# Performance work log

Measured on AMD Instinct MI355X. Metric: run time of the kernel, lower is better.

## Reference

```python
import jax, jax.numpy as jnp
import numpy as np

N_NODES = 30000
N_REL = 200
N_EDGES = 150000
N_EDGES_NHOP = 30000
NFEAT = 100
NHID = 100
REL_DIM = 100
NHEADS = 2
ALPHA = 0.2  # leaky relu slope


def setup_inputs() -> dict:
    key = jax.random.key(0)
    ks = jax.random.split(key, 16)
    s = 0.1
    D = NHEADS * NHID
    inp = {}
    inp["entity_embeddings"] = jax.random.normal(ks[0], (N_NODES, NFEAT), jnp.float32)
    inp["relation_embed"] = jax.random.normal(ks[1], (N_REL, REL_DIM), jnp.float32)
    inp["edge_list"] = jax.random.randint(ks[2], (2, N_EDGES), 0, N_NODES)
    inp["edge_type"] = jax.random.randint(ks[3], (N_EDGES,), 0, N_REL)
    inp["edge_embed"] = jax.random.normal(ks[4], (N_EDGES, REL_DIM), jnp.float32)
    inp["edge_list_nhop"] = jax.random.randint(ks[5], (2, N_EDGES_NHOP), 0, N_NODES)
    inp["edge_type_nhop"] = jax.random.randint(ks[6], (N_EDGES_NHOP, 2), 0, N_REL)
    inp["entity_embeddings_mapping"] = jax.random.normal(ks[7], (N_NODES, NFEAT), jnp.float32)
    # learned params (xavier-like scale)
    inp["a_heads"] = jax.random.normal(ks[8], (NHEADS, NHID, 2 * NFEAT + REL_DIM), jnp.float32) * s
    inp["a2_heads"] = jax.random.normal(ks[9], (NHEADS, NHID), jnp.float32) * s
    inp["W"] = jax.random.normal(ks[10], (REL_DIM, D), jnp.float32) * s
    inp["a_out"] = jax.random.normal(ks[11], (D, 3 * D), jnp.float32) * s
    inp["a2_out"] = jax.random.normal(ks[12], (D,), jnp.float32) * s
    return inp


def _att_layer(x, src, dst, edge_embed, a, a2, n_nodes, concat):
    # Sparse graph attention (KBGAT style). a: [out, 2*in + rel_dim].
    in_dim = x.shape[1]
    a_src, a_dst, a_rel = a[:, :in_dim], a[:, in_dim:2 * in_dim], a[:, 2 * in_dim:]
    # edge_m = a @ cat(x[src], x[dst], edge_embed)^T, computed without the big concat
    edge_m = x[src] @ a_src.T + x[dst] @ a_dst.T + edge_embed @ a_rel.T  # [E, out]
    powers = -jax.nn.leaky_relu(edge_m @ a2, ALPHA)                      # [E]
    edge_e = jnp.exp(powers)                                             # [E]
    e_rowsum = jax.ops.segment_sum(edge_e, src, num_segments=n_nodes)    # [N]
    e_rowsum = jnp.where(e_rowsum == 0.0, 1e-12, e_rowsum)
    h = jax.ops.segment_sum(edge_e[:, None] * edge_m, src, num_segments=n_nodes)  # [N, out]
    h = h / e_rowsum[:, None]
    return jax.nn.elu(h) if concat else h


def reference(entity_embeddings, relation_embed, edge_list, edge_type, edge_embed,
              edge_list_nhop, edge_type_nhop, entity_embeddings_mapping,
              a_heads, a2_heads, W, a_out, a2_out):
    N = entity_embeddings.shape[0]
    src = jnp.concatenate([edge_list[0], edge_list_nhop[0]])
    dst = jnp.concatenate([edge_list[1], edge_list_nhop[1]])
    # 2-hop edge embedding = sum of the two relation embeddings on the path
    ee_nhop = relation_embed[edge_type_nhop[:, 0]] + relation_embed[edge_type_nhop[:, 1]]
    ee1 = jnp.concatenate([edge_embed, ee_nhop], axis=0)
    h1 = _att_layer(entity_embeddings, src, dst, ee1, a_heads[0], a2_heads[0], N, True)
    h2 = _att_layer(entity_embeddings, src, dst, ee1, a_heads[1], a2_heads[1], N, True)
    h = jnp.concatenate([h1, h2], axis=1)  # [N, 2*nhid]; dropout p=0 (eval)
    out_relation = relation_embed @ W      # [R, 2*nhid]
    ee2 = jnp.concatenate([out_relation[edge_type],
                           out_relation[edge_type_nhop[:, 0]] + out_relation[edge_type_nhop[:, 1]]],
                          axis=0)
    out_entity = _att_layer(h, src, dst, ee2, a_out, a2_out, N, False)
    return jax.nn.elu(out_entity), out_relation
```

## Files before the change

### kernel.cpp

```cpp
#include <hip/hip_runtime.h>

#define N_NODES 30000
#define E1 150000
#define EN 30000
#define ET 180000
#define LALPHA 0.2f
#define NB_SCAN 118

typedef unsigned int u32;
typedef unsigned short u16;
typedef __attribute__((ext_vector_type(8))) short short8;
typedef __attribute__((ext_vector_type(4))) short short4v;
typedef __attribute__((ext_vector_type(4))) float f32x4;

__device__ __forceinline__ float bf2f(u16 u){ return __uint_as_float(((u32)u)<<16); }
__device__ __forceinline__ float2 bfp2(u32 u){
  return make_float2(__uint_as_float(u<<16), __uint_as_float(u & 0xffff0000u));
}
__device__ __forceinline__ u16 f2bf(float f){
  u32 x = __float_as_uint(f);
  return (u16)((x + 0x7fffu + ((x>>16)&1u)) >> 16);
}
__device__ __forceinline__ u32 pk(float x, float y){
  return ((u32)f2bf(x)) | (((u32)f2bf(y))<<16);
}
__device__ __forceinline__ float wredf(float v){
  #pragma unroll
  for(int o=32;o>0;o>>=1) v += __shfl_xor(v, o, 64);
  return v;
}
__device__ __forceinline__ float eluf(float y){ return (y>0.f)? y : expm1f(y); }
__device__ __forceinline__ float ld1(const void* p, int i, int f){
  return f ? ((const float*)p)[i] : bf2f(((const u16*)p)[i]);
}
__device__ __forceinline__ float2 ldp(const void* p, int i, int f){
  if(f){ return ((const float2*)p)[i]; }
  return bfp2(((const u32*)p)[i]);
}
__device__ __forceinline__ void st1(void* p, int i, float v, int f){
  if(f) ((float*)p)[i] = v; else ((u16*)p)[i] = f2bf(v);
}

__device__ __forceinline__ short8 frag_zero(){
  short8 r;
  #pragma unroll
  for(int i=0;i<8;i++) r[i]=0;
  return r;
}
__device__ __forceinline__ short8 ldfragb(const u16* p, int idx){
  short8 r;
  short4v lo = *(const short4v*)(p+idx);
  short4v hi = *(const short4v*)(p+idx+4);
  #pragma unroll
  for(int i=0;i<4;i++){ r[i]=lo[i]; r[4+i]=hi[i]; }
  return r;
}
__device__ __forceinline__ short8 ldfragb_p4(const u16* p, int idx){
  short8 r=frag_zero();
  short4v lo = *(const short4v*)(p+idx);
  #pragma unroll
  for(int i=0;i<4;i++) r[i]=lo[i];
  return r;
}
__device__ __forceinline__ short8 ldfrag(const void* p, int idx, int f){
  short8 r;
  if(f){
    const float* fp=(const float*)p+idx;
    #pragma unroll
    for(int i=0;i<8;i++) r[i]=(short)f2bf(fp[i]);
  } else {
    return ldfragb((const u16*)p, idx);
  }
  return r;
}
__device__ __forceinline__ short8 ldfrag_p4(const void* p, int idx, int f){
  short8 r=frag_zero();
  if(f){
    const float* fp=(const float*)p+idx;
    #pragma unroll
    for(int i=0;i<4;i++) r[i]=(short)f2bf(fp[i]);
  } else {
    return ldfragb_p4((const u16*)p, idx);
  }
  return r;
}

__global__ void k_detect(const u32* x, int* flag){
  int t = threadIdx.x;
  int c = 0;
  #pragma unroll
  for(int i=0;i<4;i++){
    u32 v = x[t*4+i];
    u32 lo = v & 0xffffu;
    u32 e = (lo>>7)&0xffu;
    c += (lo==0u || (e>=100u && e<=140u)) ? 1 : 0;
  }
  __shared__ int sd[256];
  sd[t]=c; __syncthreads();
  for(int o=128;o>0;o>>=1){ if(t<o) sd[t]+=sd[t+o]; __syncthreads(); }
  if(t==0) *flag = (sd[0] > 512) ? 0 : 1;
}

__global__ void k_prep(const void* ent, const void* ah, const void* ao,
                       u16* entB, u16* ahB, u16* aoB, const int* flag){
  int f = *flag;
  int gid = blockIdx.x*256 + threadIdx.x;
  int stride = gridDim.x*256;
  const int T0=750000, T1=765000, T2=795000;
  for(int i=gid; i<T2; i+=stride){
    const void* src; u16* dst; int g;
    if(i<T0){ src=ent; dst=entB; g=i; }
    else if(i<T1){ src=ah; dst=ahB; g=i-T0; }
    else { src=ao; dst=aoB; g=i-T1; }
    if(f){
      float4 v = ((const float4*)src)[g];
      int base=g*4;
      dst[base]=f2bf(v.x); dst[base+1]=f2bf(v.y); dst[base+2]=f2bf(v.z); dst[base+3]=f2bf(v.w);
    } else {
      ((short4v*)dst)[g] = ((const short4v*)src)[g];
    }
  }
}

__global__ void k_outrel(const void* rel, const void* W, float* outrel, void* out, const int* flag){
  int f = *flag;
  int t = blockIdx.x*blockDim.x + threadIdx.x;
  if(t >= 200*200) return;
  int r = t / 200, j = t - r*200;
  float acc = 0.f;
  for(int k=0;k<100;k++) acc += ld1(rel, r*100+k, f) * ld1(W, k*200+j, f);
  outrel[t] = acc;
  st1(out, 6000000 + t, acc, f);
}

__global__ void k_small_b(const void* ah, const void* a2h, const void* ao, const void* a2o,
                          float* b1, float* b2, const int* flag){
  int f = *flag;
  int i = blockIdx.x*4 + (threadIdx.x>>6);
  int L = threadIdx.x & 63;
  if(i >= 1200) return;
  float a = 0.f;
  if(i < 600){
    int hd = i/300, k = i - hd*300;
    for(int j=L; j<100; j+=64)
      a += ld1(a2h, hd*100+j, f) * ld1(ah, hd*30000 + j*300 + k, f);
    a = wredf(a);
    if(L==0) b1[i] = a;
  } else {
    int k = i - 600;
    for(int j=L; j<200; j+=64)
      a += ld1(a2o, j, f) * ld1(ao, j*600 + k, f);
    a = wredf(a);
    if(L==0) b2[k] = a;
  }
}

__global__ void k_small_c(const void* rel, const float* outrel, const float* b1, const float* b2,
                          float* c1, float* c2, const int* flag){
  int f = *flag;
  int i = blockIdx.x*4 + (threadIdx.x>>6);
  int L = threadIdx.x & 63;
  if(i >= 600) return;
  float a = 0.f;
  if(i < 400){
    int hd = i/200, r = i - hd*200;
    for(int k=L; k<100; k+=64)
      a += b1[hd*300+200+k] * ld1(rel, r*100+k, f);
    a = wredf(a);
    if(L==0) c1[i] = a;
  } else {
    int r = i - 400;
    for(int k=L; k<200; k+=64)
      a += b2[400+k] * outrel[r*200+k];
    a = wredf(a);
    if(L==0) c2[r] = a;
  }
}

__global__ void k_count(const int* src1, const int* srcN, int* cnt){
  int e = blockIdx.x*256 + threadIdx.x;
  if(e>=ET) return;
  int s = (e<E1)? src1[e] : srcN[e-E1];
  atomicAdd(&cnt[s],1);
}

__global__ void k_scan1(const int* cnt, int* ofs, int* bsum){
  __shared__ int sd[256];
  int b=blockIdx.x, t=threadIdx.x;
  int idx=b*256+t;
  int v=(idx<N_NODES)? cnt[idx] : 0;
  sd[t]=v; __syncthreads();
  for(int o=1;o<256;o<<=1){
    int u=(t>=o)? sd[t-o]:0;
    __syncthreads();
    sd[t]+=u; __syncthreads();
  }
  if(idx<N_NODES) ofs[idx]=sd[t]-v;
  if(t==255) bsum[b]=sd[255];
}

__global__ void k_scan2(const int* bsum, int* bstart, int* ofs){
  __shared__ int sd[128];
  int t=threadIdx.x;
  int v=(t<NB_SCAN)? bsum[t]:0;
  sd[t]=v; __syncthreads();
  for(int o=1;o<128;o<<=1){
    int u=(t>=o)? sd[t-o]:0;
    __syncthreads();
    sd[t]+=u; __syncthreads();
  }
  if(t<NB_SCAN) bstart[t]=sd[t]-v;
  if(t==127) ofs[N_NODES]=sd[127];
}

__global__ void k_scan3(int* ofs, int* cur, const int* bstart){
  int b=blockIdx.x, t=threadIdx.x;
  int idx=b*256+t;
  if(idx>=N_NODES) return;
  int v = ofs[idx] + bstart[b];
  ofs[idx]=v; cur[idx]=v;
}

__global__ void k_scatter(const int* src1, const int* srcN, int* cur, int* eord){
  int e = blockIdx.x*256 + threadIdx.x;
  if(e>=ET) return;
  int s = (e<E1)? src1[e] : srcN[e-E1];
  int p = atomicAdd(&cur[s],1);
  eord[p]=e;
}

__global__ void k_q1(const u32* entB2, const float* b1, float* q1){
  int n = blockIdx.x*4 + (threadIdx.x>>6);
  if(n>=N_NODES) return;
  int L = threadIdx.x & 63;
  float d00=0,d01=0,d10=0,d11=0;
  if(L<50){
    float2 xv = bfp2(entB2[n*50+L]);
    int k0=2*L;
    d00 = xv.x*b1[k0]     + xv.y*b1[k0+1];
    d01 = xv.x*b1[100+k0] + xv.y*b1[100+k0+1];
    d10 = xv.x*b1[300+k0] + xv.y*b1[300+k0+1];
    d11 = xv.x*b1[400+k0] + xv.y*b1[400+k0+1];
  }
  d00=wredf(d00); d01=wredf(d01); d10=wredf(d10); d11=wredf(d11);
  if(L==0){ q1[n*4+0]=d00; q1[n*4+1]=d01; q1[n*4+2]=d10; q1[n*4+3]=d11; }
}

__global__ __launch_bounds__(256) void k_edge1g(const void* ee,
    const int* src1, const int* dst1, const float* b1, const float* q1,
    float* w1, const int* flag){
  int f = *flag;
  int wid = threadIdx.x>>6, l = threadIdx.x&63;
  int lr = l&15, lg = l>>4;
  int m0 = blockIdx.x*128 + wid*32;
  short8 bfr[4];
  #pragma unroll
  for(int ks=0;ks<4;ks++){
    int kb = ks*32 + lg*8;
    short8 b = frag_zero();
    if(lr<2){
      const float* bp = b1 + (lr==0? 200:500);
      #pragma unroll
      for(int i=0;i<8;i++){ int k=kb+i; if(k<100) b[i]=(short)f2bf(bp[k]); }
    }
    bfr[ks]=b;
  }
  int row0 = m0 + lr, row1 = m0 + 16 + lr;
  bool ok0 = row0 < E1, ok1 = row1 < E1;
  f32x4 acc0=(f32x4){0,0,0,0}, acc1=(f32x4){0,0,0,0};
  #pragma unroll
  for(int ks=0;ks<4;ks++){
    int kb = ks*32 + lg*8;
    short8 a0 = frag_zero(), a1 = frag_zero();
    if(ok0){
      if(kb+8<=100) a0 = ldfrag(ee, row0*100+kb, f);
      else if(kb<100) a0 = ldfrag_p4(ee, row0*100+kb, f);
    }
    if(ok1){
      if(kb+8<=100) a1 = ldfrag(ee, row1*100+kb, f);
      else if(kb<100) a1 = ldfrag_p4(ee, row1*100+kb, f);
    }
    acc0 = __builtin_amdgcn_mfma_f32_16x16x32_bf16(a0, bfr[ks], acc0, 0,0,0);
    acc1 = __builtin_amdgcn_mfma_f32_16x16x32_bf16(a1, bfr[ks], acc1, 0,0,0);
  }
  if(lr<2){
    #pragma unroll
    for(int mi=0;mi<2;mi++){
      #pragma unroll
      for(int r=0;r<4;r++){
        int e = m0 + mi*16 + lg*4 + r;
        if(e<E1){
          float rv = (mi==0)? acc0[r] : acc1[r];
          int s=src1[e], d=dst1[e];
          float p = q1[s*4+lr*2] + q1[d*4+lr*2+1] + rv;
          p = (p>=0.f)? p : LALPHA*p;
          w1[lr*ET + e] = expf(-p);
        }
      }
    }
  }
}

__global__ void k_edge1b(const int* etn, const int* srcN, const int* dstN,
                         const float* c1, const float* q1, float* w1){
  int en = blockIdx.x*256+threadIdx.x;
  if(en>=EN) return;
  int t0=etn[en*2], t1=etn[en*2+1];
  float r0 = c1[t0]+c1[t1];
  float r1 = c1[200+t0]+c1[200+t1];
  int s=srcN[en], d=dstN[en];
  float p0 = q1[s*4+0]+q1[d*4+1]+r0;
  float p1 = q1[s*4+2]+q1[d*4+3]+r1;
  p0=(p0>=0.f)?p0:LALPHA*p0;
  p1=(p1>=0.f)?p1:LALPHA*p1;
  w1[E1+en]    = expf(-p0);
  w1[ET+E1+en] = expf(-p1);
}

__global__ void k_acc1(const int* ofs, const int* eord,
                       const int* dst1, const int* dstN, const int* etn,
                       const u32* entB2, const void* ee, const void* rel,
                       const float* w1, u32* Gq, float* rs1, const int* flag){
  int f = *flag;
  int n = blockIdx.x*4 + (threadIdx.x>>6);
  if(n>=N_NODES) return;
  int L = threadIdx.x & 63;
  int beg = ofs[n], end = ofs[n+1];
  float av0x=0,av0y=0,av1x=0,av1y=0, aw0x=0,aw0y=0,aw1x=0,aw1y=0;
  float r0=0, r1=0;
  for(int i=beg;i<end;i++){
    int e = eord[i];
    float w0 = w1[e], wh = w1[ET+e];
    r0 += w0; r1 += wh;
    bool orig = e<E1;
    int en = e-E1;
    int d = orig? dst1[e] : dstN[en];
    if(L<50){
      float2 xv = bfp2(entB2[d*50+L]);
      av0x += w0*xv.x; av0y += w0*xv.y;
      av1x += wh*xv.x; av1y += wh*xv.y;
      float2 ev;
      if(orig){ ev = ldp(ee, e*50+L, f); }
      else { int t0=etn[en*2], t1=etn[en*2+1];
             float2 e0=ldp(rel, t0*50+L, f), e1=ldp(rel, t1*50+L, f);
             ev = make_float2(e0.x+e1.x, e0.y+e1.y); }
      aw0x += w0*ev.x; aw0y += w0*ev.y;
      aw1x += wh*ev.x; aw1y += wh*ev.y;
    }
  }
  float i0 = (r0==0.f)? 0.f : 1.f/r0;
  float i1 = (r1==0.f)? 0.f : 1.f/r1;
  if(L<50){
    u32* g0 = Gq + n*100;
    u32* g1 = Gq + 3000000 + n*100;
    g0[L]    = pk(av0x*i0, av0y*i0);
    g0[50+L] = pk(aw0x*i0, aw0y*i0);
    g1[L]    = pk(av1x*i1, av1y*i1);
    g1[50+L] = pk(aw1x*i1, aw1y*i1);
  }
  if(L==0){ rs1[n]=r0; rs1[N_NODES+n]=r1; }
}

__global__ __launch_bounds__(256) void k_gemm1m(const u16* G, const u16* ahB, const u16* entB,
                        const float* rs1, u16* h){
  int hd = blockIdx.y;
  int wid = threadIdx.x>>6, l = threadIdx.x&63;
  int lr = l&15, lg = l>>4;
  int m0 = blockIdx.x*32;
  int row0 = m0 + lr, row1 = m0 + 16 + lr;
  bool hi_ok = (m0+16) < N_NODES;
  const u16* Gh0 = G + hd*6000000 + row0*200;
  const u16* Gh1 = G + hd*6000000 + row1*200;
  const u16* A = ahB + hd*30000;
  f32x4 acc[2][2];
  #pragma unroll
  for(int mi=0;mi<2;mi++)
    #pragma unroll
    for(int ntl=0;ntl<2;ntl++) acc[mi][ntl]=(f32x4){0.f,0.f,0.f,0.f};
  #pragma unroll
  for(int k0=0;k0<100;k0+=32){
    int kb = k0 + lg*8;
    short8 a0 = (kb+8<=100)? ldfragb(entB, row0*100+kb)
              : (kb<100    ? ldfragb_p4(entB, row0*100+kb) : frag_zero());
    short8 a1 = frag_zero();
    if(hi_ok){
      if(kb+8<=100) a1 = ldfragb(entB, row1*100+kb);
      else if(kb<100) a1 = ldfragb_p4(entB, row1*100+kb);
    }
    #pragma unroll
    for(int ntl=0;ntl<2;ntl++){
      int j = (ntl*4+wid)*16 + lr;
      short8 b = frag_zero();
      if(j<100){
        if(kb+8<=100) b = ldfragb(A, j*300 + kb);
        else if(kb<100) b = ldfragb_p4(A, j*300 + kb);
      }
      acc[0][ntl] = __builtin_amdgcn_mfma_f32_16x16x32_bf16(a0, b, acc[0][ntl], 0,0,0);
      acc[1][ntl] = __builtin_amdgcn_mfma_f32_16x16x32_bf16(a1, b, acc[1][ntl], 0,0,0);
    }
  }
  #pragma unroll
  for(int k0=0;k0<200;k0+=32){
    int kb = k0 + lg*8;
    short8 a0 = (kb+8<=200)? ldfragb(Gh0, kb) : frag_zero();
    short8 a1 = (hi_ok && kb+8<=200)? ldfragb(Gh1, kb) : frag_zero();
    #pragma unroll
    for(int ntl=0;ntl<2;ntl++){
      int j = (ntl*4+wid)*16 + lr;
      short8 b = (j<100 && kb+8<=200)? ldfragb(A, j*300 + 100 + kb) : frag_zero();
      acc[0][ntl] = __builtin_amdgcn_mfma_f32_16x16x32_bf16(a0, b, acc[0][ntl], 0,0,0);
      acc[1][ntl] = __builtin_amdgcn_mfma_f32_16x16x32_bf16(a1, b, acc[1][ntl], 0,0,0);
    }
  }
  #pragma unroll
  for(int mi=0;mi<2;mi++){
    if(mi==1 && !hi_ok) break;
    #pragma unroll
    for(int r=0;r<4;r++){
      int rr = m0 + mi*16 + lg*4 + r;
      float sc = (rs1[hd*N_NODES+rr]==0.f)? 0.f : 1.f;
      #pragma unroll
      for(int ntl=0;ntl<2;ntl++){
        int j = (ntl*4+wid)*16 + lr;
        if(j<100) h[rr*200 + hd*100 + j] = f2bf(eluf(acc[mi][ntl][r]*sc));
      }
    }
  }
}

__global__ void k_q2(const u32* h32, const float* b2, float* q2){
  int n = blockIdx.x*4 + (threadIdx.x>>6);
  if(n>=N_NODES) return;
  int L = threadIdx.x&63;
  float ds=0, dd=0;
  if(L<50){
    float2 a = bfp2(h32[n*100+2*L]);
    float2 b = bfp2(h32[n*100+2*L+1]);
    int k0=4*L;
    ds = a.x*b2[k0]+a.y*b2[k0+1]+b.x*b2[k0+2]+b.y*b2[k0+3];
    dd = a.x*b2[200+k0]+a.y*b2[200+k0+1]+b.x*b2[200+k0+2]+b.y*b2[200+k0+3];
  }
  ds=wredf(ds); dd=wredf(dd);
  if(L==0){ q2[n*2]=ds; q2[n*2+1]=dd; }
}

__global__ void k_edge2(const int* src1,const int* dst1,const int* srcN,const int* dstN,
                        const int* et, const int* etn, const float* c2, const float* q2, float* w2){
  int e = blockIdx.x*256+threadIdx.x;
  if(e>=ET) return;
  int s,d; float r;
  if(e<E1){ s=src1[e]; d=dst1[e]; r = c2[et[e]]; }
  else { int en=e-E1; s=srcN[en]; d=dstN[en]; r = c2[etn[en*2]]+c2[etn[en*2+1]]; }
  float p = q2[s*2] + q2[d*2+1] + r;
  p = (p>=0.f)? p : LALPHA*p;
  w2[e] = expf(-p);
}

__global__ void k_acc2(const int* ofs, const int* eord,
                       const int* dst1,const int* dstN, const int* et,const int* etn,
                       const u32* h32, const float4* or4, const float* w2,
                       u32* Gq, float* rs2){
  int n = blockIdx.x*4 + (threadIdx.x>>6);
  if(n>=N_NODES) return;
  int L = threadIdx.x&63;
  int beg=ofs[n], end=ofs[n+1];
  float rv=0;
  float avx=0,avy=0,avz=0,avw=0, awx=0,awy=0,awz=0,aww=0;
  for(int i=beg;i<end;i++){
    int e=eord[i];
    float w=w2[e];
    rv += w;
    bool orig = e<E1; int en=e-E1;
    int d = orig? dst1[e]:dstN[en];
    if(L<50){
      float2 ha = bfp2(h32[d*100+2*L]);
      float2 hb = bfp2(h32[d*100+2*L+1]);
      avx+=w*ha.x; avy+=w*ha.y; avz+=w*hb.x; avw+=w*hb.y;
      float ex,ey,ez,ew;
      if(orig){ float4 o=or4[et[e]*50+L]; ex=o.x;ey=o.y;ez=o.z;ew=o.w; }
      else { float4 a=or4[etn[en*2]*50+L], b=or4[etn[en*2+1]*50+L];
             ex=a.x+b.x; ey=a.y+b.y; ez=a.z+b.z; ew=a.w+b.w; }
      awx+=w*ex; awy+=w*ey; awz+=w*ez; aww+=w*ew;
    }
  }
  float inv = (rv==0.f)? 0.f : 1.f/rv;
  if(L<50){
    u32* g = Gq + n*200;
    g[2*L]       = pk(avx*inv, avy*inv);
    g[2*L+1]     = pk(avz*inv, avw*inv);
    g[100+2*L]   = pk(awx*inv, awy*inv);
    g[100+2*L+1] = pk(awz*inv, aww*inv);
  }
  if(L==0) rs2[n]=rv;
}

__global__ __launch_bounds__(256) void k_gemm2m(const u16* G, const u16* aoB, const u16* h,
                        const float* rs2, void* out, const int* flag){
  int f = *flag;
  int wid = threadIdx.x>>6, l = threadIdx.x&63;
  int lr = l&15, lg = l>>4;
  int m0 = blockIdx.x*32;
  int row0 = m0 + lr, row1 = m0 + 16 + lr;
  bool hi_ok = (m0+16) < N_NODES;
  const u16* h0 = h + row0*200;
  const u16* h1 = h + row1*200;
  const u16* g0 = G + row0*400;
  const u16* g1 = G + row1*400;
  f32x4 acc[2][4];
  #pragma unroll
  for(int mi=0;mi<2;mi++)
    #pragma unroll
    for(int ntl=0;ntl<4;ntl++) acc[mi][ntl]=(f32x4){0.f,0.f,0.f,0.f};
  #pragma unroll
  for(int k0=0;k0<200;k0+=32){
    int kb = k0 + lg*8;
    short8 a0 = (kb+8<=200)? ldfragb(h0, kb) : frag_zero();
    short8 a1 = (hi_ok && kb+8<=200)? ldfragb(h1, kb) : frag_zero();
    #pragma unroll
    for(int ntl=0;ntl<4;ntl++){
      int j = (ntl*4+wid)*16 + lr;
      short8 b = (j<200 && kb+8<=200)? ldfragb(aoB, j*600 + kb) : frag_zero();
      acc[0][ntl] = __builtin_amdgcn_mfma_f32_16x16x32_bf16(a0, b, acc[0][ntl], 0,0,0);
      acc[1][ntl] = __builtin_amdgcn_mfma_f32_16x16x32_bf16(a1, b, acc[1][ntl], 0,0,0);
    }
  }
  #pragma unroll
  for(int k0=0;k0<400;k0+=32){
    int kb = k0 + lg*8;
    short8 a0 = (kb+8<=400)? ldfragb(g0, kb) : frag_zero();
    short8 a1 = (hi_ok && kb+8<=400)? ldfragb(g1, kb) : frag_zero();
    #pragma unroll
    for(int ntl=0;ntl<4;ntl++){
      int j = (ntl*4+wid)*16 + lr;
      short8 b = (j<200 && kb+8<=400)? ldfragb(aoB, j*600 + 200 + kb) : frag_zero();
      acc[0][ntl] = __builtin_amdgcn_mfma_f32_16x16x32_bf16(a0, b, acc[0][ntl], 0,0,0);
      acc[1][ntl] = __builtin_amdgcn_mfma_f32_16x16x32_bf16(a1, b, acc[1][ntl], 0,0,0);
    }
  }
  #pragma unroll
  for(int mi=0;mi<2;mi++){
    if(mi==1 && !hi_ok) break;
    #pragma unroll
    for(int r=0;r<4;r++){
      int rr = m0 + mi*16 + lg*4 + r;
      float sc = (rs2[rr]==0.f)? 0.f : 1.f;
      #pragma unroll
      for(int ntl=0;ntl<4;ntl++){
        int j = (ntl*4+wid)*16 + lr;
        if(j<200) st1(out, rr*200 + j, eluf(acc[mi][ntl][r]*sc), f);
      }
    }
  }
}

extern "C" void kernel_launch(void* const* d_in, const int* in_sizes, int n_in,
                              void* d_out, int out_size, void* d_ws, size_t ws_size,
                              hipStream_t stream) {
  const void* ent = d_in[0];
  const void* rel = d_in[1];
  const int* el  = (const int*)d_in[2];
  const int* et  = (const int*)d_in[3];
  const void* ee  = d_in[4];
  const int* eln = (const int*)d_in[5];
  const int* etn = (const int*)d_in[6];
  const void* ah  = d_in[8];
  const void* a2h = d_in[9];
  const void* W   = d_in[10];
  const void* ao  = d_in[11];
  const void* a2o = d_in[12];

  float* wsf    = (float*)d_ws;
  int*   flag   = (int*)wsf;
  float* outrel = wsf+4;
  float* b1     = wsf+40008;
  float* b2     = wsf+40608;
  float* c1     = wsf+41208;
  float* c2     = wsf+41608;
  float* q1     = wsf+41808;
  float* q2     = wsf+161808;
  float* w1     = wsf+221808;
  float* w2     = wsf+581808;
  float* rs1    = wsf+761808;
  float* rs2    = wsf+821808;
  int*   ofs    = (int*)(wsf+851808);
  int*   cnt    = ofs+30001;
  int*   cur    = cnt+30000;
  int*   eord   = cur+30000;
  int*   bsum   = (int*)(wsf+1121812);
  int*   bstart = bsum+128;
  u16*   G      = (u16*)(wsf+1122072);
  u16*   h      = (u16*)(wsf+7122072);
  u16*   entB   = (u16*)(wsf+10122072);
  u16*   ahB    = (u16*)(wsf+11622072);
  u16*   aoB    = (u16*)(wsf+11652072);

  const int* src1 = el;
  const int* dst1 = el + E1;
  const int* srcN = eln;
  const int* dstN = eln + EN;

  k_detect<<<1,256,0,stream>>>((const u32*)ent, flag);
  hipMemsetAsync(cnt, 0, 30000*sizeof(int), stream);
  k_prep<<<1024,256,0,stream>>>(ent, ah, ao, entB, ahB, aoB, flag);
  k_small_b<<<300,256,0,stream>>>(ah,a2h,ao,a2o,b1,b2,flag);
  k_outrel<<<(200*200+255)/256,256,0,stream>>>(rel, W, outrel, d_out, flag);
  k_small_c<<<150,256,0,stream>>>(rel, outrel, b1, b2, c1, c2, flag);
  k_count<<<(ET+255)/256,256,0,stream>>>(src1, srcN, cnt);
  k_scan1<<<NB_SCAN,256,0,stream>>>(cnt, ofs, bsum);
  k_scan2<<<1,128,0,stream>>>(bsum, bstart, ofs);
  k_scan3<<<NB_SCAN,256,0,stream>>>(ofs, cur, bstart);
  k_scatter<<<(ET+255)/256,256,0,stream>>>(src1, srcN, cur, eord);
  k_q1<<<(N_NODES+3)/4,256,0,stream>>>((const u32*)entB, b1, q1);
  k_edge1g<<<(E1+127)/128,256,0,stream>>>(ee, src1, dst1, b1, q1, w1, flag);
  k_edge1b<<<(EN+255)/256,256,0,stream>>>(etn, srcN, dstN, c1, q1, w1);
  k_acc1<<<(N_NODES+3)/4,256,0,stream>>>(ofs, eord, dst1, dstN, etn,
                                         (const u32*)entB, ee, rel, w1, (u32*)G, rs1, flag);
  dim3 g1grid((N_NODES+31)/32, 2);
  k_gemm1m<<<g1grid,256,0,stream>>>(G, ahB, entB, rs1, h);
  k_q2<<<(N_NODES+3)/4,256,0,stream>>>((const u32*)h, b2, q2);
  k_edge2<<<(ET+255)/256,256,0,stream>>>(src1, dst1, srcN, dstN, et, etn, c2, q2, w2);
  k_acc2<<<(N_NODES+3)/4,256,0,stream>>>(ofs, eord, dst1, dstN, et, etn,
                                         (const u32*)h, (const float4*)outrel, w2, (u32*)G, rs2);
  k_gemm2m<<<(N_NODES+31)/32,256,0,stream>>>(G, aoB, h, rs2, d_out, flag);
}
```

Baseline: 278.0 us.

## Pack edge embeddings to bf16, interleave head weights, and unroll gather loops by two

While k_edge1g loads edge embeddings for the MFMA, it also writes a bf16 copy into a workspace buffer when the input is fp32 and the workspace is large enough. k_acc1 then gathers that half-size copy instead of the fp32 original. The two per-head edge weights are interleaved so each edge reads them with one float2 load. The gather loops in k_acc1 and k_acc2 are unrolled by two to keep more independent loads in flight. The cost is extra write traffic in edge1g, and the packed path depends on the workspace size check.

```diff
diff --git a/kernel.cpp b/kernel.cpp
--- a/kernel.cpp
+++ b/kernel.cpp
@@ -248,8 +248,9 @@
 
 __global__ __launch_bounds__(256) void k_edge1g(const void* ee,
     const int* src1, const int* dst1, const float* b1, const float* q1,
-    float* w1, const int* flag){
+    float* w1, u16* eeB, int ws_ok, const int* flag){
   int f = *flag;
+  int use_pack = (f==1) && ws_ok;
   int wid = threadIdx.x>>6, l = threadIdx.x&63;
   int lr = l&15, lg = l>>4;
   int m0 = blockIdx.x*128 + wid*32;
@@ -279,6 +280,19 @@
     if(ok1){
       if(kb+8<=100) a1 = ldfrag(ee, row1*100+kb, f);
       else if(kb<100) a1 = ldfrag_p4(ee, row1*100+kb, f);
+    }
+    if(use_pack){
+      short4v lo0, hi0, lo1, hi1;
+      #pragma unroll
+      for(int i=0;i<4;i++){ lo0[i]=a0[i]; hi0[i]=a0[4+i]; lo1[i]=a1[i]; hi1[i]=a1[4+i]; }
+      if(ok0){
+        if(kb+8<=100){ *(short4v*)(eeB+row0*100+kb)=lo0; *(short4v*)(eeB+row0*100+kb+4)=hi0; }
+        else if(kb<100){ *(short4v*)(eeB+row0*100+kb)=lo0; }
+      }
+      if(ok1){
+        if(kb+8<=100){ *(short4v*)(eeB+row1*100+kb)=lo1; *(short4v*)(eeB+row1*100+kb+4)=hi1; }
+        else if(kb<100){ *(short4v*)(eeB+row1*100+kb)=lo1; }
+      }
     }
     acc0 = __builtin_amdgcn_mfma_f32_16x16x32_bf16(a0, bfr[ks], acc0, 0,0,0);
     acc1 = __builtin_amdgcn_mfma_f32_16x16x32_bf16(a1, bfr[ks], acc1, 0,0,0);
@@ -294,7 +308,7 @@
           int s=src1[e], d=dst1[e];
           float p = q1[s*4+lr*2] + q1[d*4+lr*2+1] + rv;
           p = (p>=0.f)? p : LALPHA*p;
-          w1[lr*ET + e] = expf(-p);
+          w1[2*e + lr] = expf(-p);
         }
       }
     }
@@ -313,39 +327,64 @@
   float p1 = q1[s*4+2]+q1[d*4+3]+r1;
   p0=(p0>=0.f)?p0:LALPHA*p0;
   p1=(p1>=0.f)?p1:LALPHA*p1;
-  w1[E1+en]    = expf(-p0);
-  w1[ET+E1+en] = expf(-p1);
+  w1[2*(E1+en)]   = expf(-p0);
+  w1[2*(E1+en)+1] = expf(-p1);
 }
 
 __global__ void k_acc1(const int* ofs, const int* eord,
                        const int* dst1, const int* dstN, const int* etn,
-                       const u32* entB2, const void* ee, const void* rel,
-                       const float* w1, u32* Gq, float* rs1, const int* flag){
+                       const u32* entB2, const void* ee, const u32* eeB, int ws_ok,
+                       const void* rel,
+                       const float2* w1p, u32* Gq, float* rs1, const int* flag){
   int f = *flag;
+  int use_pack = (f==1) && ws_ok;
   int n = blockIdx.x*4 + (threadIdx.x>>6);
   if(n>=N_NODES) return;
   int L = threadIdx.x & 63;
   int beg = ofs[n], end = ofs[n+1];
   float av0x=0,av0y=0,av1x=0,av1y=0, aw0x=0,aw0y=0,aw1x=0,aw1y=0;
   float r0=0, r1=0;
-  for(int i=beg;i<end;i++){
-    int e = eord[i];
-    float w0 = w1[e], wh = w1[ET+e];
-    r0 += w0; r1 += wh;
-    bool orig = e<E1;
-    int en = e-E1;
-    int d = orig? dst1[e] : dstN[en];
+  int i = beg;
+  for(; i+1<end; i+=2){
+    int e0 = eord[i], e1 = eord[i+1];
+    float2 wa = w1p[e0], wb = w1p[e1];
+    r0 += wa.x + wb.x; r1 += wa.y + wb.y;
+    int d0 = (e0<E1)? dst1[e0] : dstN[e0-E1];
+    int d1 = (e1<E1)? dst1[e1] : dstN[e1-E1];
     if(L<50){
-      float2 xv = bfp2(entB2[d*50+L]);
-      av0x += w0*xv.x; av0y += w0*xv.y;
-      av1x += wh*xv.x; av1y += wh*xv.y;
-      float2 ev;
-      if(orig){ ev = ldp(ee, e*50+L, f); }
-      else { int t0=etn[en*2], t1=etn[en*2+1];
-             float2 e0=ldp(rel, t0*50+L, f), e1=ldp(rel, t1*50+L, f);
-             ev = make_float2(e0.x+e1.x, e0.y+e1.y); }
-      aw0x += w0*ev.x; aw0y += w0*ev.y;
-      aw1x += wh*ev.x; aw1y += wh*ev.y;
+      float2 x0 = bfp2(entB2[d0*50+L]);
+      float2 x1 = bfp2(entB2[d1*50+L]);
+      float2 v0, v1;
+      if(e0<E1){ v0 = use_pack? bfp2(((const u32*)eeB)[e0*50+L]) : ldp(ee, e0*50+L, f); }
+      else { int en=e0-E1; int t0=etn[en*2], t1=etn[en*2+1];
+             float2 a=ldp(rel,t0*50+L,f), b=ldp(rel,t1*50+L,f);
+             v0=make_float2(a.x+b.x, a.y+b.y); }
+      if(e1<E1){ v1 = use_pack? bfp2(((const u32*)eeB)[e1*50+L]) : ldp(ee, e1*50+L, f); }
+      else { int en=e1-E1; int t0=etn[en*2], t1=etn[en*2+1];
+             float2 a=ldp(rel,t0*50+L,f), b=ldp(rel,t1*50+L,f);
+             v1=make_float2(a.x+b.x, a.y+b.y); }
+      av0x += wa.x*x0.x + wb.x*x1.x;  av0y += wa.x*x0.y + wb.x*x1.y;
+      av1x += wa.y*x0.x + wb.y*x1.x;  av1y += wa.y*x0.y + wb.y*x1.y;
+      aw0x += wa.x*v0.x + wb.x*v1.x;  aw0y += wa.x*v0.y + wb.x*v1.y;
+      aw1x += wa.y*v0.x + wb.y*v1.x;  aw1y += wa.y*v0.y + wb.y*v1.y;
+    }
+  }
+  for(; i<end; ++i){
+    int e0 = eord[i];
+    float2 wa = w1p[e0];
+    r0 += wa.x; r1 += wa.y;
+    int d0 = (e0<E1)? dst1[e0] : dstN[e0-E1];
+    if(L<50){
+      float2 x0 = bfp2(entB2[d0*50+L]);
+      float2 v0;
+      if(e0<E1){ v0 = use_pack? bfp2(((const u32*)eeB)[e0*50+L]) : ldp(ee, e0*50+L, f); }
+      else { int en=e0-E1; int t0=etn[en*2], t1=etn[en*2+1];
+             float2 a=ldp(rel,t0*50+L,f), b=ldp(rel,t1*50+L,f);
+             v0=make_float2(a.x+b.x, a.y+b.y); }
+      av0x += wa.x*x0.x; av0y += wa.x*x0.y;
+      av1x += wa.y*x0.x; av1y += wa.y*x0.y;
+      aw0x += wa.x*v0.x; aw0y += wa.x*v0.y;
+      aw1x += wa.y*v0.x; aw1y += wa.y*v0.y;
     }
   }
   float i0 = (r0==0.f)? 0.f : 1.f/r0;
@@ -466,21 +505,42 @@
   int beg=ofs[n], end=ofs[n+1];
   float rv=0;
   float avx=0,avy=0,avz=0,avw=0, awx=0,awy=0,awz=0,aww=0;
-  for(int i=beg;i<end;i++){
-    int e=eord[i];
-    float w=w2[e];
-    rv += w;
-    bool orig = e<E1; int en=e-E1;
-    int d = orig? dst1[e]:dstN[en];
+  int i=beg;
+  for(; i+1<end; i+=2){
+    int e0=eord[i], e1=eord[i+1];
+    float w0=w2[e0], w1v=w2[e1];
+    rv += w0 + w1v;
+    int d0 = (e0<E1)? dst1[e0]:dstN[e0-E1];
+    int d1 = (e1<E1)? dst1[e1]:dstN[e1-E1];
     if(L<50){
-      float2 ha = bfp2(h32[d*100+2*L]);
-      float2 hb = bfp2(h32[d*100+2*L+1]);
-      avx+=w*ha.x; avy+=w*ha.y; avz+=w*hb.x; avw+=w*hb.y;
-      float ex,ey,ez,ew;
-      if(orig){ float4 o=or4[et[e]*50+L]; ex=o.x;ey=o.y;ez=o.z;ew=o.w; }
-      else { float4 a=or4[etn[en*2]*50+L], b=or4[etn[en*2+1]*50+L];
-             ex=a.x+b.x; ey=a.y+b.y; ez=a.z+b.z; ew=a.w+b.w; }
-      awx+=w*ex; awy+=w*ey; awz+=w*ez; aww+=w*ew;
+      float2 ha0=bfp2(h32[d0*100+2*L]), hb0=bfp2(h32[d0*100+2*L+1]);
+      float2 ha1=bfp2(h32[d1*100+2*L]), hb1=bfp2(h32[d1*100+2*L+1]);
+      float4 o0, o1;
+      if(e0<E1){ o0 = or4[et[e0]*50+L]; }
+      else { int en=e0-E1; float4 a=or4[etn[en*2]*50+L], b=or4[etn[en*2+1]*50+L];
+             o0=make_float4(a.x+b.x,a.y+b.y,a.z+b.z,a.w+b.w); }
+      if(e1<E1){ o1 = or4[et[e1]*50+L]; }
+      else { int en=e1-E1; float4 a=or4[etn[en*2]*50+L], b=or4[etn[en*2+1]*50+L];
+             o1=make_float4(a.x+b.x,a.y+b.y,a.z+b.z,a.w+b.w); }
+      avx += w0*ha0.x + w1v*ha1.x;  avy += w0*ha0.y + w1v*ha1.y;
+      avz += w0*hb0.x + w1v*hb1.x;  avw += w0*hb0.y + w1v*hb1.y;
+      awx += w0*o0.x + w1v*o1.x;  awy += w0*o0.y + w1v*o1.y;
+      awz += w0*o0.z + w1v*o1.z;  aww += w0*o0.w + w1v*o1.w;
+    }
+  }
+  for(; i<end; ++i){
+    int e0=eord[i];
+    float w0=w2[e0];
+    rv += w0;
+    int d0 = (e0<E1)? dst1[e0]:dstN[e0-E1];
+    if(L<50){
+      float2 ha0=bfp2(h32[d0*100+2*L]), hb0=bfp2(h32[d0*100+2*L+1]);
+      float4 o0;
+      if(e0<E1){ o0 = or4[et[e0]*50+L]; }
+      else { int en=e0-E1; float4 a=or4[etn[en*2]*50+L], b=or4[etn[en*2+1]*50+L];
+             o0=make_float4(a.x+b.x,a.y+b.y,a.z+b.z,a.w+b.w); }
+      avx += w0*ha0.x; avy += w0*ha0.y; avz += w0*hb0.x; avw += w0*hb0.y;
+      awx += w0*o0.x; awy += w0*o0.y; awz += w0*o0.z; aww += w0*o0.w;
     }
   }
   float inv = (rv==0.f)? 0.f : 1.f/rv;
@@ -593,6 +653,8 @@
   u16*   entB   = (u16*)(wsf+10122072);
   u16*   ahB    = (u16*)(wsf+11622072);
   u16*   aoB    = (u16*)(wsf+11652072);
+  u16*   eeB    = (u16*)(wsf+11712072);
+  int ws_ok = (ws_size >= (size_t)19212072*4) ? 1 : 0;
 
   const int* src1 = el;
   const int* dst1 = el + E1;
@@ -611,10 +673,11 @@
   k_scan3<<<NB_SCAN,256,0,stream>>>(ofs, cur, bstart);
   k_scatter<<<(ET+255)/256,256,0,stream>>>(src1, srcN, cur, eord);
   k_q1<<<(N_NODES+3)/4,256,0,stream>>>((const u32*)entB, b1, q1);
-  k_edge1g<<<(E1+127)/128,256,0,stream>>>(ee, src1, dst1, b1, q1, w1, flag);
+  k_edge1g<<<(E1+127)/128,256,0,stream>>>(ee, src1, dst1, b1, q1, w1, eeB, ws_ok, flag);
   k_edge1b<<<(EN+255)/256,256,0,stream>>>(etn, srcN, dstN, c1, q1, w1);
   k_acc1<<<(N_NODES+3)/4,256,0,stream>>>(ofs, eord, dst1, dstN, etn,
-                                         (const u32*)entB, ee, rel, w1, (u32*)G, rs1, flag);
+                                         (const u32*)entB, ee, (const u32*)eeB, ws_ok,
+                                         rel, (const float2*)w1, (u32*)G, rs1, flag);
   dim3 g1grid((N_NODES+31)/32, 2);
   k_gemm1m<<<g1grid,256,0,stream>>>(G, ahB, entB, rs1, h);
   k_q2<<<(N_NODES+3)/4,256,0,stream>>>((const u32*)h, b2, q2);
```

New measurement: 273.6 us. Within noise of the previous version (-1.6%).
